# Performance work log

Hardware: AMD Instinct MI355X
Metric: run time of the kernel (lower is better)

Reference implementation:

```python
import jax, jax.numpy as jnp
import numpy as np

THRESHOLD = 2.0 / 3.0


def _quantize_1_58_bit(weight):
    """BitNet b1.58: ternary {-1,0,+1} * scale, scale = mean(|w|) clamped."""
    scale = jnp.clip(jnp.mean(jnp.abs(weight)), 1e-5, 1000.0)
    weight_norm = jnp.clip(weight / scale, -10.0, 10.0)
    q = jnp.where(weight_norm > THRESHOLD, 1.0,
                  jnp.where(weight_norm < -THRESHOLD, -1.0, 0.0)).astype(weight.dtype)
    return q, scale


def setup_inputs() -> dict:
    key = jax.random.key(0)
    k1, k2 = jax.random.split(key)
    B, S, D_IN, D_OUT = 4, 2048, 4096, 4096
    x = jax.random.normal(k1, (B, S, D_IN), dtype=jnp.float32)
    weight = jax.random.normal(k2, (D_OUT, D_IN), dtype=jnp.float32)
    bias = jnp.zeros((D_OUT,), dtype=jnp.float32)
    return {"x": x, "weight": weight, "bias": bias}


def reference(x, weight, bias):
    # Training-path forward value == eval-path forward value:
    # dequantized ternary weight, F.linear semantics (x @ W.T + b).
    q, scale = _quantize_1_58_bit(weight)
    weight_q = q * scale  # [out, in]
    out = jnp.einsum('bsi,oi->bso', x, weight_q) + bias
    return out
```

## Files before the change

### kernel.cpp

```cpp
#include <hip/hip_runtime.h>
#include <hip/hip_bf16.h>
#include <stdint.h>


#define BM 128
#define BN 128
#define BK 64

typedef __bf16 bf16x8 __attribute__((ext_vector_type(8)));
typedef float f32x4 __attribute__((ext_vector_type(4)));

__device__ __forceinline__ unsigned short f2bf_rne(float f) {
  union { float f; unsigned int u; } v; v.f = f;
  unsigned int u = v.u;
  u += 0x7FFFu + ((u >> 16) & 1u);
  return (unsigned short)(u >> 16);
}

__global__ void absum_kernel(const float4* __restrict__ w, int n4,
                             double* __restrict__ out) {
  float s = 0.f;
  for (int i = blockIdx.x * blockDim.x + threadIdx.x; i < n4;
       i += gridDim.x * blockDim.x) {
    float4 v = w[i];
    s += fabsf(v.x) + fabsf(v.y) + fabsf(v.z) + fabsf(v.w);
  }
#pragma unroll
  for (int off = 32; off > 0; off >>= 1) s += __shfl_down(s, off);
  __shared__ float partial[4];
  if ((threadIdx.x & 63) == 0) partial[threadIdx.x >> 6] = s;
  __syncthreads();
  if (threadIdx.x == 0)
    atomicAdd(out, (double)(partial[0] + partial[1] + partial[2] + partial[3]));
}

__global__ void quant_kernel(const float4* __restrict__ w, int n4,
                             const double* __restrict__ sum, double inv_cnt,
                             ushort4* __restrict__ q) {
  float scale = (float)fmin(fmax(sum[0] * inv_cnt, 1e-5), 1000.0);
  const float T = 2.0f / 3.0f;
  for (int i = blockIdx.x * blockDim.x + threadIdx.x; i < n4;
       i += gridDim.x * blockDim.x) {
    float4 v = w[i];
    ushort4 o;
    float nx = v.x / scale, ny = v.y / scale, nz = v.z / scale, nw = v.w / scale;
    o.x = (nx > T) ? 0x3F80u : ((nx < -T) ? 0xBF80u : 0u);
    o.y = (ny > T) ? 0x3F80u : ((ny < -T) ? 0xBF80u : 0u);
    o.z = (nz > T) ? 0x3F80u : ((nz < -T) ? 0xBF80u : 0u);
    o.w = (nw > T) ? 0x3F80u : ((nw < -T) ? 0xBF80u : 0u);
    q[i] = o;
  }
}

__global__ void xcvt_kernel(const float4* __restrict__ x, int n4,
                            ushort4* __restrict__ xb) {
  for (int i = blockIdx.x * blockDim.x + threadIdx.x; i < n4;
       i += gridDim.x * blockDim.x) {
    float4 v = x[i];
    ushort4 o;
    o.x = f2bf_rne(v.x);
    o.y = f2bf_rne(v.y);
    o.z = f2bf_rne(v.z);
    o.w = f2bf_rne(v.w);
    xb[i] = o;
  }
}

__global__ void gemm_kernel(const ushort* __restrict__ xb,
                            const ushort* __restrict__ qb,
                            const float* __restrict__ bias,
                            const double* __restrict__ sum,
                            float* __restrict__ out,
                            int M, int N, int K, double inv_cnt) {
  __shared__ __align__(16) ushort As[BM * BK];
  __shared__ __align__(16) ushort Bs[BN * BK];

  const int t = threadIdx.x;
  const int wave = t >> 6;
  const int lane = t & 63;
  const int m0 = blockIdx.y * BM;
  const int n0 = blockIdx.x * BN;

  const int wr = (wave >> 1) * 64;
  const int wc = (wave & 1) * 64;
  const int lm = lane & 15;
  const int lk = lane >> 4;

  const int srow = lane >> 3;
  const int scol = (lane & 7) * 8;
  const ushort* ag = xb + (size_t)(m0 + wave * 32 + srow) * K + scol;
  const ushort* bg = qb + (size_t)(n0 + wave * 32 + srow) * K + scol;
  ushort* al = &As[(wave * 32) * BK];
  ushort* bl = &Bs[(wave * 32) * BK];

  f32x4 acc[4][4] = {};

  for (int k0 = 0; k0 < K; k0 += BK) {
#pragma unroll
    for (int s = 0; s < 4; ++s) {
      __builtin_amdgcn_global_load_lds(
          (const __attribute__((address_space(1))) void*)(ag + (size_t)s * 8 * K),
          (__attribute__((address_space(3))) void*)(al + s * 8 * BK), 16, 0, 0);
      __builtin_amdgcn_global_load_lds(
          (const __attribute__((address_space(1))) void*)(bg + (size_t)s * 8 * K),
          (__attribute__((address_space(3))) void*)(bl + s * 8 * BK), 16, 0, 0);
    }
    __syncthreads();

#pragma unroll
    for (int ks = 0; ks < 2; ++ks) {
      bf16x8 af[4], bf[4];
#pragma unroll
      for (int i = 0; i < 4; ++i)
        af[i] = *(const bf16x8*)&As[(wr + i * 16 + lm) * BK + ks * 32 + lk * 8];
#pragma unroll
      for (int j = 0; j < 4; ++j)
        bf[j] = *(const bf16x8*)&Bs[(wc + j * 16 + lm) * BK + ks * 32 + lk * 8];
#pragma unroll
      for (int i = 0; i < 4; ++i)
#pragma unroll
        for (int j = 0; j < 4; ++j)
          acc[i][j] = __builtin_amdgcn_mfma_f32_16x16x32_bf16(af[i], bf[j],
                                                             acc[i][j], 0, 0, 0);
    }
    __syncthreads();
    ag += BK;
    bg += BK;
  }

  float scale = (float)fmin(fmax(sum[0] * inv_cnt, 1e-5), 1000.0);

#pragma unroll
  for (int j = 0; j < 4; ++j) {
    const int col = n0 + wc + j * 16 + lm;
    const float bv = bias[col];
#pragma unroll
    for (int i = 0; i < 4; ++i) {
      const int row = m0 + wr + i * 16 + lk * 4;
      float* op = out + (size_t)row * N + col;
#pragma unroll
      for (int r = 0; r < 4; ++r)
        op[(size_t)r * N] = acc[i][j][r] * scale + bv;
    }
  }
}

extern "C" void kernel_launch(void* const* d_in, const int* in_sizes, int n_in,
                              void* d_out, int out_size, void* d_ws,
                              size_t ws_size, hipStream_t stream) {
  const float* x = (const float*)d_in[0];
  const float* w = (const float*)d_in[1];
  const float* bias = (const float*)d_in[2];
  float* out = (float*)d_out;

  const int DOUT = in_sizes[2];
  const int DIN = in_sizes[1] / DOUT;
  const int M = in_sizes[0] / DIN;
  const int N = DOUT, K = DIN;

  char* ws = (char*)d_ws;
  double* sum = (double*)ws;
  ushort* xb = (ushort*)(ws + 256);
  ushort* qb = (ushort*)(ws + 256 + (size_t)M * K * 2);

  const double inv_cnt = 1.0 / ((double)N * (double)K);

  hipMemsetAsync(d_ws, 0, 8, stream);

  const int wn4 = (N * K) / 4;
  absum_kernel<<<1024, 256, 0, stream>>>((const float4*)w, wn4, sum);
  quant_kernel<<<2048, 256, 0, stream>>>((const float4*)w, wn4, sum, inv_cnt,
                                         (ushort4*)qb);
  const int xn4 = (M * K) / 4;
  xcvt_kernel<<<4096, 256, 0, stream>>>((const float4*)x, xn4, (ushort4*)xb);

  dim3 grid(N / BN, M / BM);
  gemm_kernel<<<grid, 256, 0, stream>>>(xb, qb, bias, sum, out, M, N, K,
                                        inv_cnt);
}
```

Baseline: 566.2 us.

## Double-buffer GEMM LDS tiles with XOR swizzle and two-pass deterministic absum

The GEMM now uses two LDS buffers with BK reduced to 32. The next tile is prefetched via global_load_lds while MFMAs run on the current one, so only one barrier per iteration is needed. LDS row chunks are XOR-swizzled to cut bank conflicts on fragment reads. The atomic double absum plus memset is replaced by a two-kernel partial reduction that writes a precomputed scale, and grid sizes for the quant and convert kernels are changed. The smaller BK halves the MFMA work per barrier, and the prefetch relies on the single barrier to order the writes correctly.

Result: slower. 632.1 us (+11.7%).

```diff
diff --git a/kernel.cpp b/kernel.cpp
--- a/kernel.cpp
+++ b/kernel.cpp
@@ -5,7 +5,7 @@
 
 #define BM 128
 #define BN 128
-#define BK 64
+#define BK 32
 
 typedef __bf16 bf16x8 __attribute__((ext_vector_type(8)));
 typedef float f32x4 __attribute__((ext_vector_type(4)));
@@ -17,8 +17,8 @@
   return (unsigned short)(u >> 16);
 }
 
-__global__ void absum_kernel(const float4* __restrict__ w, int n4,
-                             double* __restrict__ out) {
+__global__ void absum_p1(const float4* __restrict__ w, int n4,
+                         float* __restrict__ partials) {
   float s = 0.f;
   for (int i = blockIdx.x * blockDim.x + threadIdx.x; i < n4;
        i += gridDim.x * blockDim.x) {
@@ -26,18 +26,31 @@
     s += fabsf(v.x) + fabsf(v.y) + fabsf(v.z) + fabsf(v.w);
   }
 #pragma unroll
-  for (int off = 32; off > 0; off >>= 1) s += __shfl_down(s, off);
-  __shared__ float partial[4];
-  if ((threadIdx.x & 63) == 0) partial[threadIdx.x >> 6] = s;
+  for (int o = 32; o > 0; o >>= 1) s += __shfl_down(s, o);
+  __shared__ float p[4];
+  if ((threadIdx.x & 63) == 0) p[threadIdx.x >> 6] = s;
   __syncthreads();
-  if (threadIdx.x == 0)
-    atomicAdd(out, (double)(partial[0] + partial[1] + partial[2] + partial[3]));
+  if (threadIdx.x == 0) partials[blockIdx.x] = p[0] + p[1] + p[2] + p[3];
+}
+
+__global__ void absum_p2(const float* __restrict__ partials, int n,
+                         double inv_cnt, float* __restrict__ scale_out) {
+  double s = (threadIdx.x < n) ? (double)partials[threadIdx.x] : 0.0;
+#pragma unroll
+  for (int o = 32; o > 0; o >>= 1) s += __shfl_down(s, o);
+  __shared__ double p[4];
+  if ((threadIdx.x & 63) == 0) p[threadIdx.x >> 6] = s;
+  __syncthreads();
+  if (threadIdx.x == 0) {
+    double m = (p[0] + p[1] + p[2] + p[3]) * inv_cnt;
+    scale_out[0] = (float)fmin(fmax(m, 1e-5), 1000.0);
+  }
 }
 
 __global__ void quant_kernel(const float4* __restrict__ w, int n4,
-                             const double* __restrict__ sum, double inv_cnt,
+                             const float* __restrict__ scale_p,
                              ushort4* __restrict__ q) {
-  float scale = (float)fmin(fmax(sum[0] * inv_cnt, 1e-5), 1000.0);
+  const float scale = scale_p[0];
   const float T = 2.0f / 3.0f;
   for (int i = blockIdx.x * blockDim.x + threadIdx.x; i < n4;
        i += gridDim.x * blockDim.x) {
@@ -66,14 +79,15 @@
   }
 }
 
-__global__ void gemm_kernel(const ushort* __restrict__ xb,
-                            const ushort* __restrict__ qb,
-                            const float* __restrict__ bias,
-                            const double* __restrict__ sum,
-                            float* __restrict__ out,
-                            int M, int N, int K, double inv_cnt) {
-  __shared__ __align__(16) ushort As[BM * BK];
-  __shared__ __align__(16) ushort Bs[BN * BK];
+__global__ __launch_bounds__(256) void gemm_kernel(
+    const ushort* __restrict__ xb,
+    const ushort* __restrict__ qb,
+    const float* __restrict__ bias,
+    const float* __restrict__ scale_p,
+    float* __restrict__ out,
+    int M, int N, int K) {
+  __shared__ __align__(16) ushort As[2][BM * BK];
+  __shared__ __align__(16) ushort Bs[2][BN * BK];
 
   const int t = threadIdx.x;
   const int wave = t >> 6;
@@ -86,49 +100,71 @@
   const int lm = lane & 15;
   const int lk = lane >> 4;
 
-  const int srow = lane >> 3;
-  const int scol = (lane & 7) * 8;
-  const ushort* ag = xb + (size_t)(m0 + wave * 32 + srow) * K + scol;
-  const ushort* bg = qb + (size_t)(n0 + wave * 32 + srow) * K + scol;
-  ushort* al = &As[(wave * 32) * BK];
-  ushort* bl = &Bs[(wave * 32) * BK];
+  const int srow = lane >> 2;
+  const int gchunk = (lane & 3) ^ (srow & 3);
+  const ushort* ag = xb + (size_t)(m0 + wave * 32 + srow) * K + gchunk * 8;
+  const ushort* bg = qb + (size_t)(n0 + wave * 32 + srow) * K + gchunk * 8;
+  const int lbase = (wave * 32) * BK;
 
   f32x4 acc[4][4] = {};
 
+#pragma unroll
+  for (int s = 0; s < 2; ++s) {
+    __builtin_amdgcn_global_load_lds(
+        (const __attribute__((address_space(1))) void*)(ag + (size_t)s * 16 * K),
+        (__attribute__((address_space(3))) void*)(&As[0][lbase + s * 16 * BK]),
+        16, 0, 0);
+    __builtin_amdgcn_global_load_lds(
+        (const __attribute__((address_space(1))) void*)(bg + (size_t)s * 16 * K),
+        (__attribute__((address_space(3))) void*)(&Bs[0][lbase + s * 16 * BK]),
+        16, 0, 0);
+  }
+  ag += BK;
+  bg += BK;
+
+  int par = 0;
   for (int k0 = 0; k0 < K; k0 += BK) {
-#pragma unroll
-    for (int s = 0; s < 4; ++s) {
-      __builtin_amdgcn_global_load_lds(
-          (const __attribute__((address_space(1))) void*)(ag + (size_t)s * 8 * K),
-          (__attribute__((address_space(3))) void*)(al + s * 8 * BK), 16, 0, 0);
-      __builtin_amdgcn_global_load_lds(
-          (const __attribute__((address_space(1))) void*)(bg + (size_t)s * 8 * K),
-          (__attribute__((address_space(3))) void*)(bl + s * 8 * BK), 16, 0, 0);
-    }
     __syncthreads();
-
-#pragma unroll
-    for (int ks = 0; ks < 2; ++ks) {
-      bf16x8 af[4], bf[4];
-#pragma unroll
-      for (int i = 0; i < 4; ++i)
-        af[i] = *(const bf16x8*)&As[(wr + i * 16 + lm) * BK + ks * 32 + lk * 8];
+    if (k0 + BK < K) {
+      const int nxt = par ^ 1;
+#pragma unroll
+      for (int s = 0; s < 2; ++s) {
+        __builtin_amdgcn_global_load_lds(
+            (const __attribute__((address_space(1))) void*)(ag + (size_t)s * 16 * K),
+            (__attribute__((address_space(3))) void*)(&As[nxt][lbase + s * 16 * BK]),
+            16, 0, 0);
+        __builtin_amdgcn_global_load_lds(
+            (const __attribute__((address_space(1))) void*)(bg + (size_t)s * 16 * K),
+            (__attribute__((address_space(3))) void*)(&Bs[nxt][lbase + s * 16 * BK]),
+            16, 0, 0);
+      }
+      ag += BK;
+      bg += BK;
+    }
+
+    bf16x8 af[4], bf[4];
+#pragma unroll
+    for (int i = 0; i < 4; ++i) {
+      const int row = wr + i * 16 + lm;
+      const int slot = lk ^ (row & 3);
+      af[i] = *(const bf16x8*)&As[par][row * BK + slot * 8];
+    }
+#pragma unroll
+    for (int j = 0; j < 4; ++j) {
+      const int row = wc + j * 16 + lm;
+      const int slot = lk ^ (row & 3);
+      bf[j] = *(const bf16x8*)&Bs[par][row * BK + slot * 8];
+    }
+#pragma unroll
+    for (int i = 0; i < 4; ++i)
 #pragma unroll
       for (int j = 0; j < 4; ++j)
-        bf[j] = *(const bf16x8*)&Bs[(wc + j * 16 + lm) * BK + ks * 32 + lk * 8];
-#pragma unroll
-      for (int i = 0; i < 4; ++i)
-#pragma unroll
-        for (int j = 0; j < 4; ++j)
-          acc[i][j] = __builtin_amdgcn_mfma_f32_16x16x32_bf16(af[i], bf[j],
-                                                             acc[i][j], 0, 0, 0);
-    }
-    __syncthreads();
-    ag += BK;
-    bg += BK;
-  }
-
-  float scale = (float)fmin(fmax(sum[0] * inv_cnt, 1e-5), 1000.0);
+        acc[i][j] = __builtin_amdgcn_mfma_f32_16x16x32_bf16(af[i], bf[j],
+                                                            acc[i][j], 0, 0, 0);
+    par ^= 1;
+  }
+
+  const float scale = scale_p[0];
 
 #pragma unroll
   for (int j = 0; j < 4; ++j) {
@@ -159,22 +195,21 @@
   const int N = DOUT, K = DIN;
 
   char* ws = (char*)d_ws;
-  double* sum = (double*)ws;
-  ushort* xb = (ushort*)(ws + 256);
-  ushort* qb = (ushort*)(ws + 256 + (size_t)M * K * 2);
+  float* scale_p = (float*)ws;
+  float* partials = (float*)(ws + 1024);
+  ushort* xb = (ushort*)(ws + 8192);
+  ushort* qb = (ushort*)(ws + 8192 + (size_t)M * K * 2);
 
   const double inv_cnt = 1.0 / ((double)N * (double)K);
 
-  hipMemsetAsync(d_ws, 0, 8, stream);
-
   const int wn4 = (N * K) / 4;
-  absum_kernel<<<1024, 256, 0, stream>>>((const float4*)w, wn4, sum);
-  quant_kernel<<<2048, 256, 0, stream>>>((const float4*)w, wn4, sum, inv_cnt,
+  absum_p1<<<256, 256, 0, stream>>>((const float4*)w, wn4, partials);
+  absum_p2<<<1, 256, 0, stream>>>(partials, 256, inv_cnt, scale_p);
+  quant_kernel<<<4096, 256, 0, stream>>>((const float4*)w, wn4, scale_p,
                                          (ushort4*)qb);
   const int xn4 = (M * K) / 4;
-  xcvt_kernel<<<4096, 256, 0, stream>>>((const float4*)x, xn4, (ushort4*)xb);
+  xcvt_kernel<<<8192, 256, 0, stream>>>((const float4*)x, xn4, (ushort4*)xb);
 
   dim3 grid(N / BN, M / BM);
-  gemm_kernel<<<grid, 256, 0, stream>>>(xb, qb, bias, sum, out, M, N, K,
-                                        inv_cnt);
-}
+  gemm_kernel<<<grid, 256, 0, stream>>>(xb, qb, bias, scale_p, out, M, N, K);
+}
```
